# Kernel tuning notes

Hardware: AMD Instinct MI355X
Metric: run time of the kernel (lower is better)

The kernel has to match this reference:

```python
import jax, jax.numpy as jnp
import numpy as np

VOCAB, EMB, HID, T, B = 50000, 300, 1024, 512, 64


def setup_inputs() -> dict:
    key = jax.random.key(0)
    ks = jax.random.split(key, 12)
    s_in = 1.0 / np.sqrt(HID)  # torch nn.RNN init scale
    return {
        "x": jax.random.randint(ks[0], (B, T), 0, VOCAB),
        "emb": jax.random.normal(ks[1], (VOCAB, EMB), jnp.float32),
        "W_ih0": jax.random.uniform(ks[2], (HID, EMB), jnp.float32, -s_in, s_in),
        "W_hh0": jax.random.uniform(ks[3], (HID, HID), jnp.float32, -s_in, s_in),
        "b_ih0": jax.random.uniform(ks[4], (HID,), jnp.float32, -s_in, s_in),
        "b_hh0": jax.random.uniform(ks[5], (HID,), jnp.float32, -s_in, s_in),
        "W_ih1": jax.random.uniform(ks[6], (HID, HID), jnp.float32, -s_in, s_in),
        "W_hh1": jax.random.uniform(ks[7], (HID, HID), jnp.float32, -s_in, s_in),
        "b_ih1": jax.random.uniform(ks[8], (HID,), jnp.float32, -s_in, s_in),
        "b_hh1": jax.random.uniform(ks[9], (HID,), jnp.float32, -s_in, s_in),
        "W_fc": jax.random.uniform(ks[10], (1, HID), jnp.float32, -s_in, s_in),
        "b_fc": jax.random.uniform(ks[11], (1,), jnp.float32, -s_in, s_in),
    }


def _rnn_layer(x, W_ih, W_hh, b_ih, b_hh):
    # x: [B, T, in]; precompute input projection for all timesteps (one big GEMM)
    pre = jnp.einsum('bti,hi->bth', x, W_ih) + b_ih  # [B, T, H]
    h0 = jnp.zeros((x.shape[0], W_hh.shape[0]), x.dtype)

    def step(h, p_t):
        h_new = jnp.tanh(p_t + h @ W_hh.T + b_hh)
        return h_new, h_new

    _, hs = jax.lax.scan(step, h0, jnp.swapaxes(pre, 0, 1))  # [T, B, H]
    return jnp.swapaxes(hs, 0, 1)  # [B, T, H]


def reference(x, emb, W_ih0, W_hh0, b_ih0, b_hh0, W_ih1, W_hh1, b_ih1, b_hh1, W_fc, b_fc):
    e = emb[x]                                   # [B, T, EMB] embedding lookup
    h1 = _rnn_layer(e, W_ih0, W_hh0, b_ih0, b_hh0)   # layer 0
    h2 = _rnn_layer(h1, W_ih1, W_hh1, b_ih1, b_hh1)  # layer 1
    last = h2[:, -1, :]                          # [B, H]
    return jax.nn.sigmoid(last @ W_fc.T + b_fc)  # [B, 1]
```

## Files before the change

### kernel.cpp

```cpp
#include <hip/hip_runtime.h>
#include <hip/hip_bf16.h>

#define VOCAB 50000
#define EMB   300
#define HID   1024
#define TT    512
#define BB    64


typedef __attribute__((ext_vector_type(8))) short short8;
typedef __attribute__((ext_vector_type(4))) float floatx4;

__device__ inline float b2f(unsigned int u) {
    union { unsigned int i; float f; } v; v.i = u << 16; return v.f;
}
__device__ inline unsigned short f2b(float f) {
    __hip_bfloat16 h = __float2bfloat16(f);
    return *reinterpret_cast<unsigned short*>(&h);
}

#define WAIT_VM16(N, A) asm volatile("s_waitcnt vmcnt(" #N ")"              \
    : "+v"((A)[0]), "+v"((A)[1]), "+v"((A)[2]), "+v"((A)[3]),               \
      "+v"((A)[4]), "+v"((A)[5]), "+v"((A)[6]), "+v"((A)[7]),               \
      "+v"((A)[8]), "+v"((A)[9]), "+v"((A)[10]), "+v"((A)[11]),             \
      "+v"((A)[12]), "+v"((A)[13]), "+v"((A)[14]), "+v"((A)[15])            \
    :: "memory")

__device__ inline int detect_mode256(const void* W, int tid, int* modeSh)
{
    const unsigned short* p = (const unsigned short*)W;
    int bad = 0;
    for (int i = tid; i < 1024; i += 256) {
        float v = b2f(p[2 * i]);
        if (!(v > -0.5f && v < 0.5f)) bad++;
    }
    for (int off = 32; off; off >>= 1) bad += __shfl_down(bad, off);
    if ((tid & 63) == 0) modeSh[tid >> 6] = bad;
    return 0;
}

__global__ __launch_bounds__(256)
void proj_kernel(const int*  __restrict__ xidx,
                 const void* __restrict__ emb,
                 const void* __restrict__ W,
                 const void* __restrict__ bias,
                 unsigned short* __restrict__ C,
                 int* __restrict__ ctl)
{
    const int t   = blockIdx.x;
    const int tid = threadIdx.x;
    __shared__ unsigned short eT[64 * 328];
    __shared__ unsigned short Wl[16 * 328];
    __shared__ __align__(16) unsigned short oT[1024];
    __shared__ int xqL[64];
    __shared__ int modeSh[4];

    if (t == 0) {
        for (int i = 64 + tid; i < 64 + 2048; i += 256) ctl[i] = 0;
    }
    if (tid < 64) xqL[tid] = xidx[tid * TT + t];
    for (int i = tid; i < 64 * 28; i += 256) {
        int b = i / 28, c = 300 + i % 28;
        eT[b * 328 + c] = 0;
    }
    for (int i = tid; i < 16 * 28; i += 256) {
        int nl = i / 28, c = 300 + i % 28;
        Wl[nl * 328 + c] = 0;
    }
    detect_mode256(W, tid, modeSh);
    __syncthreads();
    const int mode = (modeSh[0] + modeSh[1] + modeSh[2] + modeSh[3]) > 16;

    if (mode) {
        for (int i = tid; i < 64 * 75; i += 256) {
            int b = i / 75, seg = i % 75;
            const float* src = (const float*)emb
                             + (size_t)xqL[b] * EMB + seg * 4;
            float4 f = *(const float4*)src;
            unsigned short* d = &eT[b * 328 + seg * 4];
            d[0] = f2b(f.x); d[1] = f2b(f.y); d[2] = f2b(f.z); d[3] = f2b(f.w);
        }
    } else {
        for (int i = tid; i < 64 * 75; i += 256) {
            int b = i / 75, seg = i % 75;
            const unsigned short* src = (const unsigned short*)emb
                                      + (size_t)xqL[b] * EMB + seg * 4;
            *(uint2*)&eT[b * 328 + seg * 4] = *(const uint2*)src;
        }
    }

    const int wave = tid >> 6, lane = tid & 63;
    const int quad = lane >> 4, ln = lane & 15;

    for (int nb = 0; nb < 64; ++nb) {
        __syncthreads();
        if (mode) {
            const float* Wf = (const float*)W;
            for (int i = tid; i < 16 * 75; i += 256) {
                int nl = i / 75, seg = i % 75;
                float4 f = *(const float4*)(Wf + (size_t)(nb * 16 + nl) * EMB + seg * 4);
                unsigned short* d = &Wl[nl * 328 + seg * 4];
                d[0] = f2b(f.x); d[1] = f2b(f.y); d[2] = f2b(f.z); d[3] = f2b(f.w);
            }
        } else {
            const unsigned short* Wb = (const unsigned short*)W;
            for (int i = tid; i < 16 * 75; i += 256) {
                int nl = i / 75, seg = i % 75;
                *(uint2*)&Wl[nl * 328 + seg * 4] =
                    *(const uint2*)(Wb + (size_t)(nb * 16 + nl) * EMB + seg * 4);
            }
        }
        __syncthreads();

        floatx4 acc = {0.f, 0.f, 0.f, 0.f};
        #pragma unroll
        for (int kk = 0; kk < 10; ++kk) {
            int k = kk * 32 + quad * 8;
            short8 a = *(const short8*)&eT[(wave * 16 + ln) * 328 + k];
            short8 b = *(const short8*)&Wl[ln * 328 + k];
            acc = __builtin_amdgcn_mfma_f32_16x16x32_bf16(a, b, acc, 0, 0, 0);
        }
        const int col = nb * 16 + ln;
        const float bvf = mode ? ((const float*)bias)[col]
                               : b2f(((const unsigned short*)bias)[col]);
        oT[(wave * 16 + quad * 4 + 0) * 16 + ln] = f2b(acc[0] + bvf);
        oT[(wave * 16 + quad * 4 + 1) * 16 + ln] = f2b(acc[1] + bvf);
        oT[(wave * 16 + quad * 4 + 2) * 16 + ln] = f2b(acc[2] + bvf);
        oT[(wave * 16 + quad * 4 + 3) * 16 + ln] = f2b(acc[3] + bvf);
        __syncthreads();
        if (tid < 128) {
            short8 hv = *(const short8*)&oT[tid * 8];
            *(short8*)(C + ((size_t)t * 64 + nb) * 1024 + tid * 8) = hv;
        }
    }
}

__global__ __launch_bounds__(256)
void scan2_kernel(unsigned short* __restrict__ preB,
                  unsigned short* __restrict__ h1B,
                  unsigned short* __restrict__ h2B,
                  const void* __restrict__ Whh0, const void* __restrict__ bhh0,
                  const void* __restrict__ Wih1, const void* __restrict__ bih1,
                  const void* __restrict__ Whh1, const void* __restrict__ bhh1,
                  int* __restrict__ ctl)
{
    const int gbx  = blockIdx.x;
    const int L    = gbx >> 6;
    const int bx   = gbx & 63;
    const int n0   = bx * 16;
    int* flagsA    = ctl + 64;
    int* flagsSelf = ctl + (L ? 64 + 1024 : 64);
    unsigned short* hB = L ? h2B : h1B;
    const void* Whh  = L ? Whh1 : Whh0;
    const void* bhhv = L ? bhh1 : bhh0;

    __shared__ unsigned short Wl[16 * 1032];
    __shared__ unsigned short Wn[16 * 1032];
    __shared__ __align__(16) unsigned short hTile[1024];
    __shared__ __align__(16) unsigned short pTile[1024];
    __shared__ int modeSh[4];
    const int tid = threadIdx.x;

    detect_mode256(Whh, tid, modeSh);
    __syncthreads();
    const int mode = (modeSh[0] + modeSh[1] + modeSh[2] + modeSh[3]) > 16;

    if (mode) {
        const float* Wf = (const float*)Whh;
        for (int i = tid; i < 16 * 256; i += 256) {
            int nl = i >> 8, c = i & 255;
            float4 f = *(const float4*)(Wf + ((size_t)(n0 + nl) << 10) + c * 4);
            unsigned short* d = &Wl[nl * 1032 + c * 4];
            d[0] = f2b(f.x); d[1] = f2b(f.y); d[2] = f2b(f.z); d[3] = f2b(f.w);
        }
        if (L == 0) {
            const float* Wg = (const float*)Wih1;
            for (int i = tid; i < 16 * 256; i += 256) {
                int nl = i >> 8, c = i & 255;
                float4 f = *(const float4*)(Wg + ((size_t)(n0 + nl) << 10) + c * 4);
                unsigned short* d = &Wn[nl * 1032 + c * 4];
                d[0] = f2b(f.x); d[1] = f2b(f.y); d[2] = f2b(f.z); d[3] = f2b(f.w);
            }
        }
    } else {
        const unsigned short* Wb = (const unsigned short*)Whh;
        for (int i = tid; i < 16 * 128; i += 256) {
            int nl = i >> 7, c = i & 127;
            *(short8*)&Wl[nl * 1032 + c * 8] =
                *(const short8*)(Wb + ((size_t)(n0 + nl) << 10) + c * 8);
        }
        if (L == 0) {
            const unsigned short* Wg = (const unsigned short*)Wih1;
            for (int i = tid; i < 16 * 128; i += 256) {
                int nl = i >> 7, c = i & 127;
                *(short8*)&Wn[nl * 1032 + c * 8] =
                    *(const short8*)(Wg + ((size_t)(n0 + nl) << 10) + c * 8);
            }
        }
    }
    __syncthreads();

    const int wave = tid >> 6, lane = tid & 63;
    const int quad = lane >> 4, ln = lane & 15;
    const int brow = wave * 16 + ln;
    const int ncol = n0 + ln;
    const float bvf = mode ? ((const float*)bhhv)[ncol]
                           : b2f(((const unsigned short*)bhhv)[ncol]);
    const float bnf = (L == 0)
        ? (mode ? ((const float*)bih1)[ncol]
                : b2f(((const unsigned short*)bih1)[ncol]))
        : 0.f;
    const int b0 = wave * 16 + quad * 4;
    const unsigned short* wl = &Wl[ln * 1032 + quad * 8];
    const unsigned short* wn = &Wn[ln * 1032 + quad * 8];
    const int hoff = (quad >> 1) * 1024 + brow * 16 + (quad & 1) * 8;

    for (int t = 0; t < TT; ++t) {
        const unsigned short* pp = preB + (size_t)t * 65536 + (size_t)bx * 1024
                                        + (size_t)b0 * 16 + ln;
        unsigned int pr0, pr1, pr2, pr3;
        floatx4 acc  = {0.f, 0.f, 0.f, 0.f};
        floatx4 acc2 = {0.f, 0.f, 0.f, 0.f};

        if (L == 0) {
            pr0 = pp[0]; pr1 = pp[16]; pr2 = pp[32]; pr3 = pp[48];
            if (t > 0) {
                short8 a[32];
                const unsigned short* hp = hB + (size_t)((t - 1) & 1) * 65536 + hoff;
                #pragma unroll
                for (int kk = 0; kk < 32; ++kk)
                    asm volatile("global_load_dwordx4 %0, %1, off sc1"
                                 : "=v"(a[kk])
                                 : "v"(hp + (size_t)kk * 2048) : "memory");
                WAIT_VM16(16, a);
                #pragma unroll
                for (int kk = 0; kk < 16; ++kk) {
                    short8 b  = *(const short8*)(wl + kk * 32);
                    short8 bn = *(const short8*)(wn + kk * 32);
                    acc  = __builtin_amdgcn_mfma_f32_16x16x32_bf16(a[kk], b,  acc,  0, 0, 0);
                    acc2 = __builtin_amdgcn_mfma_f32_16x16x32_bf16(a[kk], bn, acc2, 0, 0, 0);
                }
                WAIT_VM16(0, (a + 16));
                #pragma unroll
                for (int kk = 16; kk < 32; ++kk) {
                    short8 b  = *(const short8*)(wl + kk * 32);
                    short8 bn = *(const short8*)(wn + kk * 32);
                    acc  = __builtin_amdgcn_mfma_f32_16x16x32_bf16(a[kk], b,  acc,  0, 0, 0);
                    acc2 = __builtin_amdgcn_mfma_f32_16x16x32_bf16(a[kk], bn, acc2, 0, 0, 0);
                }
            }
        } else {
            {
                const int* fp = &flagsA[bx * 16];
                for (;;) {
                    int v;
                    asm volatile("global_load_dword %0, %1, off sc1\n\t"
                                 "s_waitcnt vmcnt(0)"
                                 : "=v"(v) : "v"(fp) : "memory");
                    if (v >= t + 2) break;
                    asm volatile("s_sleep 2");
                }
            }
            if (t > 0) {
                short8 a[32];
                const unsigned short* hp = hB + (size_t)((t - 1) & 1) * 65536 + hoff;
                #pragma unroll
                for (int kk = 0; kk < 32; ++kk)
                    asm volatile("global_load_dwordx4 %0, %1, off sc1"
                                 : "=v"(a[kk])
                                 : "v"(hp + (size_t)kk * 2048) : "memory");
                WAIT_VM16(16, a);
                #pragma unroll
                for (int kk = 0; kk < 16; ++kk) {
                    short8 b = *(const short8*)(wl + kk * 32);
                    acc = __builtin_amdgcn_mfma_f32_16x16x32_bf16(a[kk], b, acc, 0, 0, 0);
                }
                asm volatile("global_load_ushort %0, %1, off sc1"
                             : "=v"(pr0) : "v"(pp) : "memory");
                asm volatile("global_load_ushort %0, %1, off offset:32 sc1"
                             : "=v"(pr1) : "v"(pp) : "memory");
                asm volatile("global_load_ushort %0, %1, off offset:64 sc1"
                             : "=v"(pr2) : "v"(pp) : "memory");
                asm volatile("global_load_ushort %0, %1, off offset:96 sc1"
                             : "=v"(pr3) : "v"(pp) : "memory");
                WAIT_VM16(4, (a + 16));
                #pragma unroll
                for (int kk = 16; kk < 32; ++kk) {
                    short8 b = *(const short8*)(wl + kk * 32);
                    acc = __builtin_amdgcn_mfma_f32_16x16x32_bf16(a[kk], b, acc, 0, 0, 0);
                }
            } else {
                asm volatile("global_load_ushort %0, %1, off sc1"
                             : "=v"(pr0) : "v"(pp) : "memory");
                asm volatile("global_load_ushort %0, %1, off offset:32 sc1"
                             : "=v"(pr1) : "v"(pp) : "memory");
                asm volatile("global_load_ushort %0, %1, off offset:64 sc1"
                             : "=v"(pr2) : "v"(pp) : "memory");
                asm volatile("global_load_ushort %0, %1, off offset:96 sc1"
                             : "=v"(pr3) : "v"(pp) : "memory");
            }
            asm volatile("s_waitcnt vmcnt(0)"
                         : "+v"(pr0), "+v"(pr1), "+v"(pr2), "+v"(pr3) :: "memory");
        }

        hTile[(b0 + 0) * 16 + ln] = f2b(tanhf(acc[0] + b2f(pr0) + bvf));
        hTile[(b0 + 1) * 16 + ln] = f2b(tanhf(acc[1] + b2f(pr1) + bvf));
        hTile[(b0 + 2) * 16 + ln] = f2b(tanhf(acc[2] + b2f(pr2) + bvf));
        hTile[(b0 + 3) * 16 + ln] = f2b(tanhf(acc[3] + b2f(pr3) + bvf));
        if (L == 0 && t > 0) {
            pTile[(b0 + 0) * 16 + ln] = f2b(acc2[0] + bnf);
            pTile[(b0 + 1) * 16 + ln] = f2b(acc2[1] + bnf);
            pTile[(b0 + 2) * 16 + ln] = f2b(acc2[2] + bnf);
            pTile[(b0 + 3) * 16 + ln] = f2b(acc2[3] + bnf);
        }
        __syncthreads();
        if (tid < 128) {
            short8 hv = *(const short8*)&hTile[tid * 8];
            asm volatile("global_store_dwordx4 %0, %1, off sc1"
                         :: "v"(hB + (size_t)(t & 1) * 65536 + (size_t)bx * 1024 + tid * 8),
                            "v"(hv) : "memory");
            if (L == 0 && t > 0) {
                short8 pv = *(const short8*)&pTile[tid * 8];
                asm volatile("global_store_dwordx4 %0, %1, off sc1"
                             :: "v"(preB + (size_t)(t - 1) * 65536 + (size_t)bx * 1024 + tid * 8),
                                "v"(pv) : "memory");
            }
        }
        if (t < TT - 1) {
            asm volatile("s_waitcnt vmcnt(0)" ::: "memory");
            __syncthreads();
            if (tid == 0) {
                int tv = t + 1;
                asm volatile("global_store_dword %0, %1, off sc1"
                             :: "v"(&flagsSelf[bx * 16]), "v"(tv) : "memory");
            }
            if (tid < 64) {
                const int* fp = &flagsSelf[tid * 16];
                for (;;) {
                    int v;
                    asm volatile("global_load_dword %0, %1, off sc1\n\t"
                                 "s_waitcnt vmcnt(0)"
                                 : "=v"(v) : "v"(fp) : "memory");
                    if (!__any(v < t + 1)) break;
                    asm volatile("s_sleep 1");
                }
            }
            __syncthreads();
        }
    }

    if (L == 0) {
        asm volatile("s_waitcnt vmcnt(0)" ::: "memory");
        __syncthreads();
        if (tid == 0) {
            int tv = TT;
            asm volatile("global_store_dword %0, %1, off sc1"
                         :: "v"(&flagsSelf[bx * 16]), "v"(tv) : "memory");
        }
        if (tid < 64) {
            const int* fp = &flagsSelf[tid * 16];
            for (;;) {
                int v;
                asm volatile("global_load_dword %0, %1, off sc1\n\t"
                             "s_waitcnt vmcnt(0)"
                             : "=v"(v) : "v"(fp) : "memory");
                if (!__any(v < TT)) break;
                asm volatile("s_sleep 1");
            }
        }
        __syncthreads();

        const unsigned short* hp = hB + (size_t)((TT - 1) & 1) * 65536 + hoff;
        short8 a[32];
        floatx4 acc2 = {0.f, 0.f, 0.f, 0.f};
        #pragma unroll
        for (int kk = 0; kk < 32; ++kk)
            asm volatile("global_load_dwordx4 %0, %1, off sc1"
                         : "=v"(a[kk])
                         : "v"(hp + (size_t)kk * 2048) : "memory");
        WAIT_VM16(16, a);
        #pragma unroll
        for (int kk = 0; kk < 16; ++kk) {
            short8 bn = *(const short8*)(wn + kk * 32);
            acc2 = __builtin_amdgcn_mfma_f32_16x16x32_bf16(a[kk], bn, acc2, 0, 0, 0);
        }
        WAIT_VM16(0, (a + 16));
        #pragma unroll
        for (int kk = 16; kk < 32; ++kk) {
            short8 bn = *(const short8*)(wn + kk * 32);
            acc2 = __builtin_amdgcn_mfma_f32_16x16x32_bf16(a[kk], bn, acc2, 0, 0, 0);
        }
        pTile[(b0 + 0) * 16 + ln] = f2b(acc2[0] + bnf);
        pTile[(b0 + 1) * 16 + ln] = f2b(acc2[1] + bnf);
        pTile[(b0 + 2) * 16 + ln] = f2b(acc2[2] + bnf);
        pTile[(b0 + 3) * 16 + ln] = f2b(acc2[3] + bnf);
        __syncthreads();
        if (tid < 128) {
            short8 pv = *(const short8*)&pTile[tid * 8];
            asm volatile("global_store_dwordx4 %0, %1, off sc1"
                         :: "v"(preB + (size_t)(TT - 1) * 65536 + (size_t)bx * 1024 + tid * 8),
                            "v"(pv) : "memory");
        }
        asm volatile("s_waitcnt vmcnt(0)" ::: "memory");
        __syncthreads();
        if (tid == 0) {
            int tv = TT + 1;
            asm volatile("global_store_dword %0, %1, off sc1"
                         :: "v"(&flagsSelf[bx * 16]), "v"(tv) : "memory");
        }
    }
}

__global__ __launch_bounds__(1024)
void fc_kernel(const unsigned short* __restrict__ h,
               const void* __restrict__ Wfc,
               const void* __restrict__ bfc,
               const void* __restrict__ WhhD,
               float* __restrict__ out)
{
    const int tid = threadIdx.x;
    __shared__ int modeSh[16];
    {
        const unsigned short* p = (const unsigned short*)WhhD;
        int bad = 0;
        if (tid < 1024) {
            float v = b2f(p[2 * tid]);
            if (!(v > -0.5f && v < 0.5f)) bad++;
        }
        for (int off = 32; off; off >>= 1) bad += __shfl_down(bad, off);
        if ((tid & 63) == 0) modeSh[tid >> 6] = bad;
    }
    __syncthreads();
    int modeSum = 0;
    for (int w = 0; w < 16; ++w) modeSum += modeSh[w];
    const int mode = modeSum > 16;

    const int b = tid >> 4, sub = tid & 15;
    const unsigned short* hr = h + (size_t)((TT - 1) & 1) * 65536 + b * 16 + sub;
    float s = 0.f;
    for (int j = 0; j < 64; ++j) {
        float w = mode ? ((const float*)Wfc)[j * 16 + sub]
                       : b2f(((const unsigned short*)Wfc)[j * 16 + sub]);
        s += b2f(hr[(size_t)j * 1024]) * w;
    }
    for (int off = 8; off; off >>= 1)
        s += __shfl_down(s, off, 16);
    if (sub == 0) {
        float bv = mode ? ((const float*)bfc)[0]
                        : b2f(((const unsigned short*)bfc)[0]);
        out[b] = 1.f / (1.f + expf(-(s + bv)));
    }
}

extern "C" void kernel_launch(void* const* d_in, const int* in_sizes, int n_in,
                              void* d_out, int out_size, void* d_ws, size_t ws_size,
                              hipStream_t stream)
{
    const int*  x    = (const int*)d_in[0];
    const void* emb  = d_in[1];
    const void* Wih0 = d_in[2];
    const void* Whh0 = d_in[3];
    const void* bih0 = d_in[4];
    const void* bhh0 = d_in[5];
    const void* Wih1 = d_in[6];
    const void* Whh1 = d_in[7];
    const void* bih1 = d_in[8];
    const void* bhh1 = d_in[9];
    const void* Wfc  = d_in[10];
    const void* bfc  = d_in[11];
    float* out = (float*)d_out;

    char* ws = (char*)d_ws;
    int*            ctl  = (int*)ws;
    unsigned short* pre  = (unsigned short*)(ws + 16384);
    unsigned short* h1   = (unsigned short*)(ws + 16384 + (size_t)67108864);
    unsigned short* h2   = h1 + 2 * 65536;

    proj_kernel<<<dim3(512), dim3(256), 0, stream>>>(
        x, emb, Wih0, bih0, pre, ctl);
    scan2_kernel<<<dim3(128), dim3(256), 0, stream>>>(
        pre, h1, h2, Whh0, bhh0, Wih1, bih1, Whh1, bhh1, ctl);
    fc_kernel<<<dim3(1), dim3(1024), 0, stream>>>(h2, Wfc, bfc, Whh1, out);
}
```

Measured before the change: 2.404 ms.

## Halve persistent scan blocks, each owning 32 hidden columns instead of 16

The persistent two-layer scan kernel now runs 64 blocks (32 per layer) instead of 128, and each block computes 32 output columns with two MFMA accumulator chains per weight matrix. Weight slices in LDS double to 32 rows, h/pre tiles double, and the per-step flag polling only checks 32 peers instead of 64. The goal is to cut grid-wide synchronization cost and redundant h loads per step (each loaded h tile feeds twice as many MFMAs), at the price of more serial work per block per step and higher LDS use.

```diff
diff --git a/kernel.cpp b/kernel.cpp
--- a/kernel.cpp
+++ b/kernel.cpp
@@ -25,6 +25,10 @@
       "+v"((A)[8]), "+v"((A)[9]), "+v"((A)[10]), "+v"((A)[11]),             \
       "+v"((A)[12]), "+v"((A)[13]), "+v"((A)[14]), "+v"((A)[15])            \
     :: "memory")
+
+#define WAIT_PR8(P) asm volatile("s_waitcnt vmcnt(0)"                        \
+    : "+v"((P)[0]), "+v"((P)[1]), "+v"((P)[2]), "+v"((P)[3]),               \
+      "+v"((P)[4]), "+v"((P)[5]), "+v"((P)[6]), "+v"((P)[7]) :: "memory")
 
 __device__ inline int detect_mode256(const void* W, int tid, int* modeSh)
 {
@@ -135,7 +139,7 @@
     }
 }
 
-__global__ __launch_bounds__(256)
+__global__ __launch_bounds__(256, 1)
 void scan2_kernel(unsigned short* __restrict__ preB,
                   unsigned short* __restrict__ h1B,
                   unsigned short* __restrict__ h2B,
@@ -145,19 +149,19 @@
                   int* __restrict__ ctl)
 {
     const int gbx  = blockIdx.x;
-    const int L    = gbx >> 6;
-    const int bx   = gbx & 63;
-    const int n0   = bx * 16;
+    const int L    = gbx >> 5;
+    const int bx   = gbx & 31;
+    const int n0   = bx * 32;
     int* flagsA    = ctl + 64;
     int* flagsSelf = ctl + (L ? 64 + 1024 : 64);
     unsigned short* hB = L ? h2B : h1B;
     const void* Whh  = L ? Whh1 : Whh0;
     const void* bhhv = L ? bhh1 : bhh0;
 
-    __shared__ unsigned short Wl[16 * 1032];
-    __shared__ unsigned short Wn[16 * 1032];
-    __shared__ __align__(16) unsigned short hTile[1024];
-    __shared__ __align__(16) unsigned short pTile[1024];
+    __shared__ unsigned short Wl[32 * 1032];
+    __shared__ unsigned short Wn[32 * 1032];
+    __shared__ __align__(16) unsigned short hTile[2048];
+    __shared__ __align__(16) unsigned short pTile[2048];
     __shared__ int modeSh[4];
     const int tid = threadIdx.x;
 
@@ -167,7 +171,7 @@
 
     if (mode) {
         const float* Wf = (const float*)Whh;
-        for (int i = tid; i < 16 * 256; i += 256) {
+        for (int i = tid; i < 32 * 256; i += 256) {
             int nl = i >> 8, c = i & 255;
             float4 f = *(const float4*)(Wf + ((size_t)(n0 + nl) << 10) + c * 4);
             unsigned short* d = &Wl[nl * 1032 + c * 4];
@@ -175,7 +179,7 @@
         }
         if (L == 0) {
             const float* Wg = (const float*)Wih1;
-            for (int i = tid; i < 16 * 256; i += 256) {
+            for (int i = tid; i < 32 * 256; i += 256) {
                 int nl = i >> 8, c = i & 255;
                 float4 f = *(const float4*)(Wg + ((size_t)(n0 + nl) << 10) + c * 4);
                 unsigned short* d = &Wn[nl * 1032 + c * 4];
@@ -184,14 +188,14 @@
         }
     } else {
         const unsigned short* Wb = (const unsigned short*)Whh;
-        for (int i = tid; i < 16 * 128; i += 256) {
+        for (int i = tid; i < 32 * 128; i += 256) {
             int nl = i >> 7, c = i & 127;
             *(short8*)&Wl[nl * 1032 + c * 8] =
                 *(const short8*)(Wb + ((size_t)(n0 + nl) << 10) + c * 8);
         }
         if (L == 0) {
             const unsigned short* Wg = (const unsigned short*)Wih1;
-            for (int i = tid; i < 16 * 128; i += 256) {
+            for (int i = tid; i < 32 * 128; i += 256) {
                 int nl = i >> 7, c = i & 127;
                 *(short8*)&Wn[nl * 1032 + c * 8] =
                     *(const short8*)(Wg + ((size_t)(n0 + nl) << 10) + c * 8);
@@ -203,27 +207,38 @@
     const int wave = tid >> 6, lane = tid & 63;
     const int quad = lane >> 4, ln = lane & 15;
     const int brow = wave * 16 + ln;
-    const int ncol = n0 + ln;
-    const float bvf = mode ? ((const float*)bhhv)[ncol]
-                           : b2f(((const unsigned short*)bhhv)[ncol]);
-    const float bnf = (L == 0)
-        ? (mode ? ((const float*)bih1)[ncol]
-                : b2f(((const unsigned short*)bih1)[ncol]))
-        : 0.f;
+    const int nc0 = n0 + ln, nc1 = n0 + 16 + ln;
+    const float bvf0 = mode ? ((const float*)bhhv)[nc0]
+                            : b2f(((const unsigned short*)bhhv)[nc0]);
+    const float bvf1 = mode ? ((const float*)bhhv)[nc1]
+                            : b2f(((const unsigned short*)bhhv)[nc1]);
+    const float bnf0 = (L == 0)
+        ? (mode ? ((const float*)bih1)[nc0]
+                : b2f(((const unsigned short*)bih1)[nc0])) : 0.f;
+    const float bnf1 = (L == 0)
+        ? (mode ? ((const float*)bih1)[nc1]
+                : b2f(((const unsigned short*)bih1)[nc1])) : 0.f;
     const int b0 = wave * 16 + quad * 4;
-    const unsigned short* wl = &Wl[ln * 1032 + quad * 8];
-    const unsigned short* wn = &Wn[ln * 1032 + quad * 8];
+    const unsigned short* wl0 = &Wl[ln * 1032 + quad * 8];
+    const unsigned short* wl1 = wl0 + 16 * 1032;
+    const unsigned short* wn0 = &Wn[ln * 1032 + quad * 8];
+    const unsigned short* wn1 = wn0 + 16 * 1032;
     const int hoff = (quad >> 1) * 1024 + brow * 16 + (quad & 1) * 8;
 
     for (int t = 0; t < TT; ++t) {
-        const unsigned short* pp = preB + (size_t)t * 65536 + (size_t)bx * 1024
-                                        + (size_t)b0 * 16 + ln;
-        unsigned int pr0, pr1, pr2, pr3;
-        floatx4 acc  = {0.f, 0.f, 0.f, 0.f};
-        floatx4 acc2 = {0.f, 0.f, 0.f, 0.f};
+        const unsigned short* pp0 = preB + (size_t)t * 65536
+                                  + (size_t)(2 * bx) * 1024
+                                  + (size_t)b0 * 16 + ln;
+        const unsigned short* pp1 = pp0 + 1024;
+        unsigned int pr[8];
+        floatx4 acc0  = {0.f, 0.f, 0.f, 0.f};
+        floatx4 acc1  = {0.f, 0.f, 0.f, 0.f};
+        floatx4 acc20 = {0.f, 0.f, 0.f, 0.f};
+        floatx4 acc21 = {0.f, 0.f, 0.f, 0.f};
 
         if (L == 0) {
-            pr0 = pp[0]; pr1 = pp[16]; pr2 = pp[32]; pr3 = pp[48];
+            pr[0] = pp0[0]; pr[1] = pp0[16]; pr[2] = pp0[32]; pr[3] = pp0[48];
+            pr[4] = pp1[0]; pr[5] = pp1[16]; pr[6] = pp1[32]; pr[7] = pp1[48];
             if (t > 0) {
                 short8 a[32];
                 const unsigned short* hp = hB + (size_t)((t - 1) & 1) * 65536 + hoff;
@@ -235,18 +250,26 @@
                 WAIT_VM16(16, a);
                 #pragma unroll
                 for (int kk = 0; kk < 16; ++kk) {
-                    short8 b  = *(const short8*)(wl + kk * 32);
-                    short8 bn = *(const short8*)(wn + kk * 32);
-                    acc  = __builtin_amdgcn_mfma_f32_16x16x32_bf16(a[kk], b,  acc,  0, 0, 0);
-                    acc2 = __builtin_amdgcn_mfma_f32_16x16x32_bf16(a[kk], bn, acc2, 0, 0, 0);
+                    short8 b0f = *(const short8*)(wl0 + kk * 32);
+                    short8 b1f = *(const short8*)(wl1 + kk * 32);
+                    short8 n0f = *(const short8*)(wn0 + kk * 32);
+                    short8 n1f = *(const short8*)(wn1 + kk * 32);
+                    acc0  = __builtin_amdgcn_mfma_f32_16x16x32_bf16(a[kk], b0f, acc0,  0, 0, 0);
+                    acc1  = __builtin_amdgcn_mfma_f32_16x16x32_bf16(a[kk], b1f, acc1,  0, 0, 0);
+                    acc20 = __builtin_amdgcn_mfma_f32_16x16x32_bf16(a[kk], n0f, acc20, 0, 0, 0);
+                    acc21 = __builtin_amdgcn_mfma_f32_16x16x32_bf16(a[kk], n1f, acc21, 0, 0, 0);
                 }
                 WAIT_VM16(0, (a + 16));
                 #pragma unroll
                 for (int kk = 16; kk < 32; ++kk) {
-                    short8 b  = *(const short8*)(wl + kk * 32);
-                    short8 bn = *(const short8*)(wn + kk * 32);
-                    acc  = __builtin_amdgcn_mfma_f32_16x16x32_bf16(a[kk], b,  acc,  0, 0, 0);
-                    acc2 = __builtin_amdgcn_mfma_f32_16x16x32_bf16(a[kk], bn, acc2, 0, 0, 0);
+                    short8 b0f = *(const short8*)(wl0 + kk * 32);
+                    short8 b1f = *(const short8*)(wl1 + kk * 32);
+                    short8 n0f = *(const short8*)(wn0 + kk * 32);
+                    short8 n1f = *(const short8*)(wn1 + kk * 32);
+                    acc0  = __builtin_amdgcn_mfma_f32_16x16x32_bf16(a[kk], b0f, acc0,  0, 0, 0);
+                    acc1  = __builtin_amdgcn_mfma_f32_16x16x32_bf16(a[kk], b1f, acc1,  0, 0, 0);
+                    acc20 = __builtin_amdgcn_mfma_f32_16x16x32_bf16(a[kk], n0f, acc20, 0, 0, 0);
+                    acc21 = __builtin_amdgcn_mfma_f32_16x16x32_bf16(a[kk], n1f, acc21, 0, 0, 0);
                 }
             }
         } else {
@@ -272,57 +295,86 @@
                 WAIT_VM16(16, a);
                 #pragma unroll
                 for (int kk = 0; kk < 16; ++kk) {
-                    short8 b = *(const short8*)(wl + kk * 32);
-                    acc = __builtin_amdgcn_mfma_f32_16x16x32_bf16(a[kk], b, acc, 0, 0, 0);
+                    short8 b0f = *(const short8*)(wl0 + kk * 32);
+                    short8 b1f = *(const short8*)(wl1 + kk * 32);
+                    acc0 = __builtin_amdgcn_mfma_f32_16x16x32_bf16(a[kk], b0f, acc0, 0, 0, 0);
+                    acc1 = __builtin_amdgcn_mfma_f32_16x16x32_bf16(a[kk], b1f, acc1, 0, 0, 0);
                 }
                 asm volatile("global_load_ushort %0, %1, off sc1"
-                             : "=v"(pr0) : "v"(pp) : "memory");
+                             : "=v"(pr[0]) : "v"(pp0) : "memory");
                 asm volatile("global_load_ushort %0, %1, off offset:32 sc1"
-                             : "=v"(pr1) : "v"(pp) : "memory");
+                             : "=v"(pr[1]) : "v"(pp0) : "memory");
                 asm volatile("global_load_ushort %0, %1, off offset:64 sc1"
-                             : "=v"(pr2) : "v"(pp) : "memory");
+                             : "=v"(pr[2]) : "v"(pp0) : "memory");
                 asm volatile("global_load_ushort %0, %1, off offset:96 sc1"
-                             : "=v"(pr3) : "v"(pp) : "memory");
-                WAIT_VM16(4, (a + 16));
+                             : "=v"(pr[3]) : "v"(pp0) : "memory");
+                asm volatile("global_load_ushort %0, %1, off sc1"
+                             : "=v"(pr[4]) : "v"(pp1) : "memory");
+                asm volatile("global_load_ushort %0, %1, off offset:32 sc1"
+                             : "=v"(pr[5]) : "v"(pp1) : "memory");
+                asm volatile("global_load_ushort %0, %1, off offset:64 sc1"
+                             : "=v"(pr[6]) : "v"(pp1) : "memory");
+                asm volatile("global_load_ushort %0, %1, off offset:96 sc1"
+                             : "=v"(pr[7]) : "v"(pp1) : "memory");
+                WAIT_VM16(8, (a + 16));
                 #pragma unroll
                 for (int kk = 16; kk < 32; ++kk) {
-                    short8 b = *(const short8*)(wl + kk * 32);
-                    acc = __builtin_amdgcn_mfma_f32_16x16x32_bf16(a[kk], b, acc, 0, 0, 0);
+                    short8 b0f = *(const short8*)(wl0 + kk * 32);
+                    short8 b1f = *(const short8*)(wl1 + kk * 32);
+                    acc0 = __builtin_amdgcn_mfma_f32_16x16x32_bf16(a[kk], b0f, acc0, 0, 0, 0);
+                    acc1 = __builtin_amdgcn_mfma_f32_16x16x32_bf16(a[kk], b1f, acc1, 0, 0, 0);
                 }
             } else {
                 asm volatile("global_load_ushort %0, %1, off sc1"
-                             : "=v"(pr0) : "v"(pp) : "memory");
+                             : "=v"(pr[0]) : "v"(pp0) : "memory");
                 asm volatile("global_load_ushort %0, %1, off offset:32 sc1"
-                             : "=v"(pr1) : "v"(pp) : "memory");
+                             : "=v"(pr[1]) : "v"(pp0) : "memory");
                 asm volatile("global_load_ushort %0, %1, off offset:64 sc1"
-                             : "=v"(pr2) : "v"(pp) : "memory");
+                             : "=v"(pr[2]) : "v"(pp0) : "memory");
                 asm volatile("global_load_ushort %0, %1, off offset:96 sc1"
-                             : "=v"(pr3) : "v"(pp) : "memory");
-            }
-            asm volatile("s_waitcnt vmcnt(0)"
-                         : "+v"(pr0), "+v"(pr1), "+v"(pr2), "+v"(pr3) :: "memory");
-        }
-
-        hTile[(b0 + 0) * 16 + ln] = f2b(tanhf(acc[0] + b2f(pr0) + bvf));
-        hTile[(b0 + 1) * 16 + ln] = f2b(tanhf(acc[1] + b2f(pr1) + bvf));
-        hTile[(b0 + 2) * 16 + ln] = f2b(tanhf(acc[2] + b2f(pr2) + bvf));
-        hTile[(b0 + 3) * 16 + ln] = f2b(tanhf(acc[3] + b2f(pr3) + bvf));
+                             : "=v"(pr[3]) : "v"(pp0) : "memory");
+                asm volatile("global_load_ushort %0, %1, off sc1"
+                             : "=v"(pr[4]) : "v"(pp1) : "memory");
+                asm volatile("global_load_ushort %0, %1, off offset:32 sc1"
+                             : "=v"(pr[5]) : "v"(pp1) : "memory");
+                asm volatile("global_load_ushort %0, %1, off offset:64 sc1"
+                             : "=v"(pr[6]) : "v"(pp1) : "memory");
+                asm volatile("global_load_ushort %0, %1, off offset:96 sc1"
+                             : "=v"(pr[7]) : "v"(pp1) : "memory");
+            }
+            WAIT_PR8(pr);
+        }
+
+        hTile[(b0 + 0) * 16 + ln]        = f2b(tanhf(acc0[0] + b2f(pr[0]) + bvf0));
+        hTile[(b0 + 1) * 16 + ln]        = f2b(tanhf(acc0[1] + b2f(pr[1]) + bvf0));
+        hTile[(b0 + 2) * 16 + ln]        = f2b(tanhf(acc0[2] + b2f(pr[2]) + bvf0));
+        hTile[(b0 + 3) * 16 + ln]        = f2b(tanhf(acc0[3] + b2f(pr[3]) + bvf0));
+        hTile[1024 + (b0 + 0) * 16 + ln] = f2b(tanhf(acc1[0] + b2f(pr[4]) + bvf1));
+        hTile[1024 + (b0 + 1) * 16 + ln] = f2b(tanhf(acc1[1] + b2f(pr[5]) + bvf1));
+        hTile[1024 + (b0 + 2) * 16 + ln] = f2b(tanhf(acc1[2] + b2f(pr[6]) + bvf1));
+        hTile[1024 + (b0 + 3) * 16 + ln] = f2b(tanhf(acc1[3] + b2f(pr[7]) + bvf1));
         if (L == 0 && t > 0) {
-            pTile[(b0 + 0) * 16 + ln] = f2b(acc2[0] + bnf);
-            pTile[(b0 + 1) * 16 + ln] = f2b(acc2[1] + bnf);
-            pTile[(b0 + 2) * 16 + ln] = f2b(acc2[2] + bnf);
-            pTile[(b0 + 3) * 16 + ln] = f2b(acc2[3] + bnf);
-        }
-        __syncthreads();
-        if (tid < 128) {
+            pTile[(b0 + 0) * 16 + ln]        = f2b(acc20[0] + bnf0);
+            pTile[(b0 + 1) * 16 + ln]        = f2b(acc20[1] + bnf0);
+            pTile[(b0 + 2) * 16 + ln]        = f2b(acc20[2] + bnf0);
+            pTile[(b0 + 3) * 16 + ln]        = f2b(acc20[3] + bnf0);
+            pTile[1024 + (b0 + 0) * 16 + ln] = f2b(acc21[0] + bnf1);
+            pTile[1024 + (b0 + 1) * 16 + ln] = f2b(acc21[1] + bnf1);
+            pTile[1024 + (b0 + 2) * 16 + ln] = f2b(acc21[2] + bnf1);
+            pTile[1024 + (b0 + 3) * 16 + ln] = f2b(acc21[3] + bnf1);
+        }
+        __syncthreads();
+        {
             short8 hv = *(const short8*)&hTile[tid * 8];
             asm volatile("global_store_dwordx4 %0, %1, off sc1"
-                         :: "v"(hB + (size_t)(t & 1) * 65536 + (size_t)bx * 1024 + tid * 8),
+                         :: "v"(hB + (size_t)(t & 1) * 65536
+                                + (size_t)(2 * bx) * 1024 + tid * 8),
                             "v"(hv) : "memory");
             if (L == 0 && t > 0) {
                 short8 pv = *(const short8*)&pTile[tid * 8];
                 asm volatile("global_store_dwordx4 %0, %1, off sc1"
-                             :: "v"(preB + (size_t)(t - 1) * 65536 + (size_t)bx * 1024 + tid * 8),
+                             :: "v"(preB + (size_t)(t - 1) * 65536
+                                    + (size_t)(2 * bx) * 1024 + tid * 8),
                                 "v"(pv) : "memory");
             }
         }
@@ -335,12 +387,13 @@
                              :: "v"(&flagsSelf[bx * 16]), "v"(tv) : "memory");
             }
             if (tid < 64) {
-                const int* fp = &flagsSelf[tid * 16];
                 for (;;) {
-                    int v;
-                    asm volatile("global_load_dword %0, %1, off sc1\n\t"
-                                 "s_waitcnt vmcnt(0)"
-                                 : "=v"(v) : "v"(fp) : "memory");
+                    int v = 0x7fffffff;
+                    if (tid < 32) {
+                        asm volatile("global_load_dword %0, %1, off sc1\n\t"
+                                     "s_waitcnt vmcnt(0)"
+                                     : "=v"(v) : "v"(&flagsSelf[tid * 16]) : "memory");
+                    }
                     if (!__any(v < t + 1)) break;
                     asm volatile("s_sleep 1");
                 }
@@ -358,12 +411,13 @@
                          :: "v"(&flagsSelf[bx * 16]), "v"(tv) : "memory");
         }
         if (tid < 64) {
-            const int* fp = &flagsSelf[tid * 16];
             for (;;) {
-                int v;
-                asm volatile("global_load_dword %0, %1, off sc1\n\t"
-                             "s_waitcnt vmcnt(0)"
-                             : "=v"(v) : "v"(fp) : "memory");
+                int v = 0x7fffffff;
+                if (tid < 32) {
+                    asm volatile("global_load_dword %0, %1, off sc1\n\t"
+                                 "s_waitcnt vmcnt(0)"
+                                 : "=v"(v) : "v"(&flagsSelf[tid * 16]) : "memory");
+                }
                 if (!__any(v < TT)) break;
                 asm volatile("s_sleep 1");
             }
@@ -372,7 +426,8 @@
 
         const unsigned short* hp = hB + (size_t)((TT - 1) & 1) * 65536 + hoff;
         short8 a[32];
-        floatx4 acc2 = {0.f, 0.f, 0.f, 0.f};
+        floatx4 acc20 = {0.f, 0.f, 0.f, 0.f};
+        floatx4 acc21 = {0.f, 0.f, 0.f, 0.f};
         #pragma unroll
         for (int kk = 0; kk < 32; ++kk)
             asm volatile("global_load_dwordx4 %0, %1, off sc1"
@@ -381,24 +436,33 @@
         WAIT_VM16(16, a);
         #pragma unroll
         for (int kk = 0; kk < 16; ++kk) {
-            short8 bn = *(const short8*)(wn + kk * 32);
-            acc2 = __builtin_amdgcn_mfma_f32_16x16x32_bf16(a[kk], bn, acc2, 0, 0, 0);
+            short8 n0f = *(const short8*)(wn0 + kk * 32);
+            short8 n1f = *(const short8*)(wn1 + kk * 32);
+            acc20 = __builtin_amdgcn_mfma_f32_16x16x32_bf16(a[kk], n0f, acc20, 0, 0, 0);
+            acc21 = __builtin_amdgcn_mfma_f32_16x16x32_bf16(a[kk], n1f, acc21, 0, 0, 0);
         }
         WAIT_VM16(0, (a + 16));
         #pragma unroll
         for (int kk = 16; kk < 32; ++kk) {
-            short8 bn = *(const short8*)(wn + kk * 32);
-            acc2 = __builtin_amdgcn_mfma_f32_16x16x32_bf16(a[kk], bn, acc2, 0, 0, 0);
-        }
-        pTile[(b0 + 0) * 16 + ln] = f2b(acc2[0] + bnf);
-        pTile[(b0 + 1) * 16 + ln] = f2b(acc2[1] + bnf);
-        pTile[(b0 + 2) * 16 + ln] = f2b(acc2[2] + bnf);
-        pTile[(b0 + 3) * 16 + ln] = f2b(acc2[3] + bnf);
-        __syncthreads();
-        if (tid < 128) {
+            short8 n0f = *(const short8*)(wn0 + kk * 32);
+            short8 n1f = *(const short8*)(wn1 + kk * 32);
+            acc20 = __builtin_amdgcn_mfma_f32_16x16x32_bf16(a[kk], n0f, acc20, 0, 0, 0);
+            acc21 = __builtin_amdgcn_mfma_f32_16x16x32_bf16(a[kk], n1f, acc21, 0, 0, 0);
+        }
+        pTile[(b0 + 0) * 16 + ln]        = f2b(acc20[0] + bnf0);
+        pTile[(b0 + 1) * 16 + ln]        = f2b(acc20[1] + bnf0);
+        pTile[(b0 + 2) * 16 + ln]        = f2b(acc20[2] + bnf0);
+        pTile[(b0 + 3) * 16 + ln]        = f2b(acc20[3] + bnf0);
+        pTile[1024 + (b0 + 0) * 16 + ln] = f2b(acc21[0] + bnf1);
+        pTile[1024 + (b0 + 1) * 16 + ln] = f2b(acc21[1] + bnf1);
+        pTile[1024 + (b0 + 2) * 16 + ln] = f2b(acc21[2] + bnf1);
+        pTile[1024 + (b0 + 3) * 16 + ln] = f2b(acc21[3] + bnf1);
+        __syncthreads();
+        {
             short8 pv = *(const short8*)&pTile[tid * 8];
             asm volatile("global_store_dwordx4 %0, %1, off sc1"
-                         :: "v"(preB + (size_t)(TT - 1) * 65536 + (size_t)bx * 1024 + tid * 8),
+                         :: "v"(preB + (size_t)(TT - 1) * 65536
+                                + (size_t)(2 * bx) * 1024 + tid * 8),
                             "v"(pv) : "memory");
         }
         asm volatile("s_waitcnt vmcnt(0)" ::: "memory");
@@ -478,7 +542,7 @@
 
     proj_kernel<<<dim3(512), dim3(256), 0, stream>>>(
         x, emb, Wih0, bih0, pre, ctl);
-    scan2_kernel<<<dim3(128), dim3(256), 0, stream>>>(
+    scan2_kernel<<<dim3(64), dim3(256), 0, stream>>>(
         pre, h1, h2, Whh0, bhh0, Wih1, bih1, Whh1, bhh1, ctl);
     fc_kernel<<<dim3(1), dim3(1024), 0, stream>>>(h2, Wfc, bfc, Whh1, out);
 }
```

Measured after the change: 3.183 ms. 1.32x slower.
